# Kernel optimization log

Hardware: AMD Instinct MI355X
Metric: run time of the kernel (lower is better)

Reference implementation:

```python
import jax, jax.numpy as jnp
from jax import lax
import numpy as np

B, T, C, L, K, LS = 128, 64, 6625, 25, 6, 25
ALPHA, SMOOTH_TAIL, BLANK = 0.1, 0.01, 0


def setup_inputs() -> dict:
    key = jax.random.key(0)
    k1, k2, k3, k4, k5 = jax.random.split(key, 5)
    preds = jax.random.normal(k1, (B, T, C), jnp.float32)
    text = jax.random.randint(k2, (B, L), 1, C)            # labels avoid blank=0
    length = jax.random.randint(k3, (B,), 10, L + 1)       # master target lengths
    preds_size = jnp.full((B,), T, jnp.int32)              # full time length per sample
    smooth_text = jax.random.randint(k4, (B, K, LS), 1, C)
    smooth_length = jax.random.randint(k5, (B, K), 5, LS + 1)
    return dict(preds=preds, text=text, preds_size=preds_size, length=length,
                smooth_text=smooth_text, smooth_length=smooth_length)


def ctc_nll(log_probs, sample_idx, targets, input_lens, target_lens):
    """Batched CTC negative log likelihood (torch.nn.CTCLoss math, zero_infinity).
    log_probs: [T, Bsrc, C] log-softmax; sample_idx: [N] -> Bsrc (lets N targets
    share logits without materializing [T, N, C]); targets: [N, Lmax]."""
    Tt = log_probs.shape[0]
    N, Lt = targets.shape
    S = 2 * Lt + 1
    NEG = jnp.float32(-1e30)
    ext = jnp.full((N, S), BLANK, dtype=targets.dtype).at[:, 1::2].set(targets)
    ext_m2 = jnp.pad(ext[:, :-2], ((0, 0), (2, 0)), constant_values=BLANK)
    allow_skip = (ext != BLANK) & (ext != ext_m2)          # [N, S]

    def frame(lp_t):                                        # [Bsrc,C] -> [N,S]
        return jnp.take_along_axis(lp_t[sample_idx], ext, axis=1)

    lp0 = frame(log_probs[0])
    alpha = jnp.full((N, S), NEG).at[:, 0].set(lp0[:, 0]).at[:, 1].set(lp0[:, 1])

    def step(alpha, xs):
        t, lp_t = xs
        s1 = jnp.pad(alpha[:, :-1], ((0, 0), (1, 0)), constant_values=NEG)
        s2 = jnp.where(allow_skip,
                       jnp.pad(alpha[:, :-2], ((0, 0), (2, 0)), constant_values=NEG), NEG)
        m = jnp.maximum(alpha, jnp.maximum(s1, s2))
        tot = m + jnp.log(jnp.exp(alpha - m) + jnp.exp(s1 - m) + jnp.exp(s2 - m))
        new = tot + frame(lp_t)
        return jnp.where((t < input_lens)[:, None], new, alpha), None

    alpha, _ = lax.scan(step, alpha, (jnp.arange(1, Tt), log_probs[1:]))
    il = (2 * target_lens)[:, None]                         # final blank position
    a_blank = jnp.take_along_axis(alpha, il, axis=1)[:, 0]
    a_char = jnp.take_along_axis(alpha, jnp.maximum(il - 1, 0), axis=1)[:, 0]
    nll = -jnp.logaddexp(a_blank, a_char)
    return jnp.where(nll > 1e29, 0.0, nll)                  # zero_infinity


def _confidence_beam1(lp):
    """CTC prefix beam search with beam_size=1 on one sample. lp: [T, C] log-probs.
    Returns length-normalized prefix probability as the confidence score."""
    Cc = lp.shape[1]
    NEG = jnp.float32(-1e30)
    cs = jnp.arange(Cc)

    def step(state, lp_t):
        lpb, lpnb, last = state
        tot = jnp.logaddexp(lpb, lpnb)
        new_pb = tot + lp_t[BLANK]
        rep = jnp.where(last >= 0, lpnb + lp_t[jnp.maximum(last, 0)], NEG)
        keep = jnp.logaddexp(new_pb, rep)                   # keep same prefix
        ext = jnp.where(cs == last, lpb, tot) + lp_t        # extend by char c
        ext = ext.at[BLANK].set(NEG)
        best_c = jnp.argmax(ext)
        best_ext = ext[best_c]
        take_ext = best_ext > keep
        return (jnp.where(take_ext, NEG, new_pb),
                jnp.where(take_ext, best_ext, rep),
                jnp.where(take_ext, best_c.astype(jnp.int32), last)), None

    init = (jnp.float32(0.0), NEG, jnp.int32(-1))
    (lpb, lpnb, _), _ = lax.scan(step, init, lp)
    score = jnp.logaddexp(lpb, lpnb)
    return jnp.exp(score / lp.shape[0])


def reference(preds, text, preds_size, length, smooth_text, smooth_length):
    lp = jax.nn.log_softmax(preds, axis=2)                  # [B, T, C]
    lp_tbc = jnp.transpose(lp, (1, 0, 2))                   # [T, B, C]
    conf = lax.stop_gradient(jax.vmap(_confidence_beam1)(lp))  # no_grad block

    # master CTC loss (reduction='mean': nll / target_len, then batch mean)
    nll_m = ctc_nll(lp_tbc, jnp.arange(B), text, preds_size, length)
    loss_master = jnp.mean(nll_m / length.astype(lp.dtype))

    # smoothing CTC losses: K hypotheses per sample share that sample's logits
    idx_s = jnp.repeat(jnp.arange(B), K)
    nll_s = ctc_nll(lp_tbc, idx_s, smooth_text.reshape(B * K, LS),
                    jnp.full((B * K,), T, jnp.int32), smooth_length.reshape(B * K))
    loss_cal = jnp.mean((nll_s / smooth_length.reshape(-1).astype(lp.dtype)).reshape(B, K), axis=1)

    ranking = SMOOTH_TAIL + (1.0 - SMOOTH_TAIL) * (1.0 - conf) ** 2
    return loss_master + jnp.mean(ALPHA * ranking * loss_cal)
```

## Files before the change

### kernel.cpp

```cpp
#include <hip/hip_runtime.h>
#include <cstddef>

#define BB   128
#define TT   64
#define CC   6625
#define LL   25
#define KK   6
#define LSS  25
#define SS   51
#define NEG  (-1e30f)
#define FNEG (-3.4e38f)
#define PIVOT 16.0f

#define NCTC       (BB + BB * KK)
#define CTC_BLOCKS (NCTC / 4)

__device__ __forceinline__ float lae(float a, float b) {
    float m = fmaxf(a, b);
    float n = fminf(a, b);
    return m + __logf(1.0f + __expf(n - m));
}

__global__ __launch_bounds__(256, 4) void row_stats_k(
    const float* __restrict__ preds,
    float* __restrict__ lse_t, float* __restrict__ t1v, float* __restrict__ t2v,
    int* __restrict__ t1i, int* __restrict__ t2i, float* __restrict__ cal)
{
    if (blockIdx.x == 0 && threadIdx.x < BB) cal[threadIdx.x] = 0.0f;

    int wave = threadIdx.x >> 6, lane = threadIdx.x & 63;
    int r = blockIdx.x * 4 + wave;
    const float* row = preds + (size_t)r * CC;

    int h = (4 - (r & 3)) & 3;
    const float4* vp = (const float4*)(row + h);
    int nv = (CC - h) >> 2;
    int t0 = h + (nv << 2);

    float headx = (lane < h) ? row[lane] : FNEG;
    float tailx = (lane < CC - t0) ? row[t0 + lane] : FNEG;
    int   remidx = 1600 + lane;
    bool  remv = remidx < nv;
    float4 remx = vp[remv ? remidx : 0];

    float s0 = 0.0f, s1 = 0.0f, s2 = 0.0f, s3 = 0.0f;
    float v1 = FNEG, v2 = FNEG;
    int   i1 = 0x7fffffff, i2 = 0x7fffffff;

    auto top2 = [&](float x, int c) {
        bool g1 = (x > v1);
        bool g2 = (x > v2);
        v2 = g1 ? v1 : (g2 ? x : v2);
        i2 = g1 ? i1 : (g2 ? c : i2);
        v1 = g1 ? x : v1;
        i1 = g1 ? c : i1;
    };
    auto proc4 = [&](float4 x, int c) {
        s0 += __expf(x.x - PIVOT);
        s1 += __expf(x.y - PIVOT);
        s2 += __expf(x.z - PIVOT);
        s3 += __expf(x.w - PIVOT);
        top2((c == 0) ? FNEG : x.x, c);
        top2(x.y, c + 1);
        top2(x.z, c + 2);
        top2(x.w, c + 3);
    };

    float4 buf[6];
    #pragma unroll
    for (int k = 0; k < 6; ++k) buf[k] = vp[k * 64 + lane];
    #pragma unroll
    for (int k = 0; k < 25; ++k) {
        float4 x = buf[k % 6];
        if (k + 6 < 25) buf[k % 6] = vp[(k + 6) * 64 + lane];
        proc4(x, h + (k * 64 + lane) * 4);
    }

    if (lane < h) {
        s0 += __expf(headx - PIVOT);
        if (lane > 0) top2(headx, lane);
    }
    if (remv) proc4(remx, h + (remidx << 2));
    if (lane < CC - t0) {
        s0 += __expf(tailx - PIVOT);
        top2(tailx, t0 + lane);
    }

    float s = (s0 + s1) + (s2 + s3);
    for (int off = 32; off > 0; off >>= 1) {
        s += __shfl_xor(s, off);
        float w1 = __shfl_xor(v1, off); int j1 = __shfl_xor(i1, off);
        float w2 = __shfl_xor(v2, off); int j2 = __shfl_xor(i2, off);
        bool b1 = (w1 > v1) || (w1 == v1 && j1 < i1);
        bool b2a = (v1 > w2) || (v1 == w2 && i1 < j2);
        bool b2b = (w1 > v2) || (w1 == v2 && j1 < i2);
        float nv2 = b1 ? (b2a ? v1 : w2) : (b2b ? w1 : v2);
        int   ni2 = b1 ? (b2a ? i1 : j2) : (b2b ? j1 : i2);
        v1 = b1 ? w1 : v1; i1 = b1 ? j1 : i1;
        v2 = nv2; i2 = ni2;
    }

    if (lane == 0) {
        int b = r >> 6, t = r & 63;
        int tr = t * BB + b;
        lse_t[tr] = PIVOT + __logf(s);
        t1v[tr] = v1; t1i[tr] = i1;
        t2v[tr] = v2; t2i[tr] = i2;
    }
}

__global__ __launch_bounds__(256) void ctc_beam_k(
    const float* __restrict__ preds, const float* __restrict__ lse_t,
    const float* __restrict__ t1v, const float* __restrict__ t2v,
    const int* __restrict__ t1i, const int* __restrict__ t2i,
    const int* __restrict__ text, const int* __restrict__ length,
    const int* __restrict__ preds_size,
    const int* __restrict__ smooth_text, const int* __restrict__ smooth_length,
    float* __restrict__ nllm, float* __restrict__ cal, float* __restrict__ ranking)
{
    if (blockIdx.x == CTC_BLOCKS) {
        int b = threadIdx.x;
        if (b >= BB) return;
        const float* pb = preds + (size_t)b * TT * CC;

        float sum_lse = 0.0f;
        #pragma unroll 8
        for (int t = 0; t < TT; ++t) sum_lse += lse_t[t * BB + b];

        float lpb = 0.0f, lpnb = NEG;
        int last = -1;
        float pf0[8];
        #pragma unroll
        for (int i = 0; i < 8; ++i) pf0[i] = pb[(size_t)i * CC];
        float lplast_raw = 0.0f;
        for (int t = 0; t < TT; ++t) {
            int tr = t * BB + b;
            float w1 = t1v[tr]; int j1 = t1i[tr];
            float w2 = t2v[tr]; int j2 = t2i[tr];
            float lp0 = pf0[t & 7];
            if (t + 8 < TT) pf0[t & 7] = pb[(size_t)(t + 8) * CC];
            float tot = lae(lpb, lpnb);
            float new_pb = tot + lp0;
            float rep = (last >= 0) ? (lpnb + lplast_raw) : NEG;
            float keep = lae(new_pb, rep);
            float best_ext; int best_c;
            if (j1 == last) {
                float eA = lpb + w1;
                float eB = tot + w2;
                if (eA > eB || (eA == eB && last < j2)) { best_ext = eA; best_c = last; }
                else                                    { best_ext = eB; best_c = j2; }
            } else {
                best_ext = tot + w1;
                best_c = j1;
            }
            bool take = best_ext > keep;
            lpb  = take ? NEG : new_pb;
            lpnb = take ? best_ext : rep;
            last = take ? best_c : last;
            if (t + 1 < TT && last >= 0) lplast_raw = pb[(size_t)(t + 1) * CC + last];
        }
        float score = lae(lpb, lpnb) - sum_lse;
        float conf = __expf(score * (1.0f / TT));
        float om = 1.0f - conf;
        ranking[b] = 0.01f + 0.99f * om * om;
        return;
    }

    int wave = threadIdx.x >> 6, lane = threadIdx.x & 63;
    int n = blockIdx.x * 4 + wave;
    if (n >= NCTC) return;
    bool master = n < BB;
    int b, tlen, input_len;
    const int* tgt;
    if (master) {
        b = n; tgt = text + (size_t)n * LL; tlen = length[n]; input_len = preds_size[b];
    } else {
        int ns = n - BB;
        b = ns / KK; tgt = smooth_text + (size_t)ns * LSS; tlen = smooth_length[ns]; input_len = TT;
    }

    int s = lane;
    int ext = 0; bool skipok = false;
    if (s < SS && (s & 1)) {
        int li = (s - 1) >> 1;
        ext = tgt[li];
        skipok = (ext != 0) && (li == 0 || ext != tgt[li - 1]);
    }

    const float* pb = preds + (size_t)b * TT * CC;

    float sum_lse = (lane < input_len) ? lse_t[lane * BB + b] : 0.0f;
    for (int off = 32; off > 0; off >>= 1) sum_lse += __shfl_xor(sum_lse, off);

    float alpha = NEG;
    if (s < 2) alpha = pb[ext];

    float pf[8];
    #pragma unroll
    for (int i = 0; i < 8; ++i) pf[i] = pb[(size_t)(1 + i) * CC + ext];
    for (int t = 1; t < TT; ++t) {
        int slot = (t - 1) & 7;
        float lp = pf[slot];
        if (t + 8 < TT) pf[slot] = pb[(size_t)(t + 8) * CC + ext];
        float a0 = alpha;
        float a1 = __shfl_up(alpha, 1); a1 = (lane >= 1) ? a1 : NEG;
        float a2 = __shfl_up(alpha, 2); a2 = (lane >= 2 && skipok) ? a2 : NEG;
        float m = fmaxf(a0, fmaxf(a1, a2));
        float tot = m + __logf(__expf(a0 - m) + __expf(a1 - m) + __expf(a2 - m));
        float anew = tot + lp;
        alpha = (t < input_len) ? anew : alpha;
    }

    int il = 2 * tlen;
    float a_bl = __shfl(alpha, il);
    float a_ch = __shfl(alpha, il > 0 ? il - 1 : 0);
    float nll = sum_lse - lae(a_bl, a_ch);
    if (nll > 1e29f) nll = 0.0f;
    if (lane == 0) {
        float v = nll / (float)tlen;
        if (master) nllm[b] = v;
        else        atomicAdd(&cal[b], v * (1.0f / KK));
    }
}

__global__ __launch_bounds__(128) void final_k(
    const float* __restrict__ nllm, const float* __restrict__ ranking,
    const float* __restrict__ cal, float* __restrict__ out)
{
    int b = threadIdx.x;
    float v = nllm[b] + 0.1f * ranking[b] * cal[b];
    for (int off = 32; off > 0; off >>= 1) v += __shfl_xor(v, off);
    __shared__ float sv[2];
    if ((b & 63) == 0) sv[b >> 6] = v;
    __syncthreads();
    if (b == 0) out[0] = (sv[0] + sv[1]) * (1.0f / BB);
}

extern "C" void kernel_launch(void* const* d_in, const int* in_sizes, int n_in,
                              void* d_out, int out_size, void* d_ws, size_t ws_size,
                              hipStream_t stream)
{
    const float* preds         = (const float*)d_in[0];
    const int*   text          = (const int*)d_in[1];
    const int*   preds_size    = (const int*)d_in[2];
    const int*   length        = (const int*)d_in[3];
    const int*   smooth_text   = (const int*)d_in[4];
    const int*   smooth_length = (const int*)d_in[5];
    float* out = (float*)d_out;

    const int RT = BB * TT;
    float* ws     = (float*)d_ws;
    float* lse_t  = ws;
    float* t1v    = ws + RT;
    float* t2v    = ws + 2 * RT;
    int*   t1i    = (int*)(ws + 3 * RT);
    int*   t2i    = (int*)(ws + 4 * RT);
    float* ranking = ws + 5 * RT;
    float* nllm    = ranking + BB;
    float* cal     = nllm + BB;

    row_stats_k<<<RT / 4, 256, 0, stream>>>(preds, lse_t, t1v, t2v, t1i, t2i, cal);
    ctc_beam_k<<<CTC_BLOCKS + 1, 256, 0, stream>>>(preds, lse_t, t1v, t2v, t1i, t2i,
                                                   text, length, preds_size,
                                                   smooth_text, smooth_length,
                                                   nllm, cal, ranking);
    final_k<<<1, 128, 0, stream>>>(nllm, ranking, cal, out);
}
```

Measured before the change: 347.7 us.

## Process each softmax row with a full 256-thread block instead of one wave

The row statistics kernel now assigns one row per 256-thread block rather than one row per 64-lane wave. Each thread issues all seven of its float4 loads up front, and the per-wave partial sums and top-2 candidates are combined through shared memory. The goal is more memory parallelism per row and shorter per-thread serial loops. The cost is four times as many blocks, plus a __syncthreads and a serial cross-wave merge in thread 0.

```diff
diff --git a/kernel.cpp b/kernel.cpp
--- a/kernel.cpp
+++ b/kernel.cpp
@@ -26,22 +26,28 @@
     float* __restrict__ lse_t, float* __restrict__ t1v, float* __restrict__ t2v,
     int* __restrict__ t1i, int* __restrict__ t2i, float* __restrict__ cal)
 {
-    if (blockIdx.x == 0 && threadIdx.x < BB) cal[threadIdx.x] = 0.0f;
-
-    int wave = threadIdx.x >> 6, lane = threadIdx.x & 63;
-    int r = blockIdx.x * 4 + wave;
+    int r = blockIdx.x;
+    int tid = threadIdx.x;
+    if (r == 0 && tid < BB) cal[tid] = 0.0f;
+
     const float* row = preds + (size_t)r * CC;
-
     int h = (4 - (r & 3)) & 3;
     const float4* vp = (const float4*)(row + h);
     int nv = (CC - h) >> 2;
     int t0 = h + (nv << 2);
-
-    float headx = (lane < h) ? row[lane] : FNEG;
-    float tailx = (lane < CC - t0) ? row[t0 + lane] : FNEG;
-    int   remidx = 1600 + lane;
-    bool  remv = remidx < nv;
-    float4 remx = vp[remv ? remidx : 0];
+    int ntail = CC - t0;
+
+    float headx = (tid < h)     ? row[tid]       : FNEG;
+    float tailx = (tid < ntail) ? row[t0 + tid]  : FNEG;
+    int li6 = tid + 1536;
+    bool v6ok = li6 < nv;
+    float4 x0 = vp[tid];
+    float4 x1 = vp[tid + 256];
+    float4 x2 = vp[tid + 512];
+    float4 x3 = vp[tid + 768];
+    float4 x4 = vp[tid + 1024];
+    float4 x5 = vp[tid + 1280];
+    float4 x6 = vp[v6ok ? li6 : 0];
 
     float s0 = 0.0f, s1 = 0.0f, s2 = 0.0f, s3 = 0.0f;
     float v1 = FNEG, v2 = FNEG;
@@ -66,25 +72,19 @@
         top2(x.w, c + 3);
     };
 
-    float4 buf[6];
-    #pragma unroll
-    for (int k = 0; k < 6; ++k) buf[k] = vp[k * 64 + lane];
-    #pragma unroll
-    for (int k = 0; k < 25; ++k) {
-        float4 x = buf[k % 6];
-        if (k + 6 < 25) buf[k % 6] = vp[(k + 6) * 64 + lane];
-        proc4(x, h + (k * 64 + lane) * 4);
-    }
-
-    if (lane < h) {
-        s0 += __expf(headx - PIVOT);
-        if (lane > 0) top2(headx, lane);
-    }
-    if (remv) proc4(remx, h + (remidx << 2));
-    if (lane < CC - t0) {
-        s0 += __expf(tailx - PIVOT);
-        top2(tailx, t0 + lane);
-    }
+    proc4(x0, h + (tid << 2));
+    proc4(x1, h + ((tid + 256) << 2));
+    proc4(x2, h + ((tid + 512) << 2));
+    proc4(x3, h + ((tid + 768) << 2));
+    proc4(x4, h + ((tid + 1024) << 2));
+    proc4(x5, h + ((tid + 1280) << 2));
+    if (!v6ok) { x6.x = FNEG; x6.y = FNEG; x6.z = FNEG; x6.w = FNEG; }
+    proc4(x6, h + (li6 << 2));
+
+    s0 += __expf(headx - PIVOT);
+    top2((tid == 0) ? FNEG : headx, tid);
+    s0 += __expf(tailx - PIVOT);
+    top2(tailx, t0 + tid);
 
     float s = (s0 + s1) + (s2 + s3);
     for (int off = 32; off > 0; off >>= 1) {
@@ -100,7 +100,25 @@
         v2 = nv2; i2 = ni2;
     }
 
-    if (lane == 0) {
+    __shared__ float ss_[4], sv1[4], sv2[4];
+    __shared__ int   si1[4], si2[4];
+    int wave = tid >> 6, lane = tid & 63;
+    if (lane == 0) { ss_[wave] = s; sv1[wave] = v1; si1[wave] = i1; sv2[wave] = v2; si2[wave] = i2; }
+    __syncthreads();
+    if (tid == 0) {
+        for (int w = 1; w < 4; ++w) {
+            s += ss_[w];
+            float w1 = sv1[w]; int j1 = si1[w]; float w2 = sv2[w]; int j2 = si2[w];
+            bool b1 = (w1 > v1) || (w1 == v1 && j1 < i1);
+            if (b1) {
+                bool b2 = (v1 > w2) || (v1 == w2 && i1 < j2);
+                v2 = b2 ? v1 : w2; i2 = b2 ? i1 : j2;
+                v1 = w1; i1 = j1;
+            } else {
+                bool b2 = (w1 > v2) || (w1 == v2 && j1 < i2);
+                if (b2) { v2 = w1; i2 = j1; }
+            }
+        }
         int b = r >> 6, t = r & 63;
         int tr = t * BB + b;
         lse_t[tr] = PIVOT + __logf(s);
@@ -259,7 +277,7 @@
     float* nllm    = ranking + BB;
     float* cal     = nllm + BB;
 
-    row_stats_k<<<RT / 4, 256, 0, stream>>>(preds, lse_t, t1v, t2v, t1i, t2i, cal);
+    row_stats_k<<<RT, 256, 0, stream>>>(preds, lse_t, t1v, t2v, t1i, t2i, cal);
     ctc_beam_k<<<CTC_BLOCKS + 1, 256, 0, stream>>>(preds, lse_t, t1v, t2v, t1i, t2i,
                                                    text, length, preds_size,
                                                    smooth_text, smooth_length,
```

Result: no change. 346.6 us (-0.3%).
